# Kernel optimization log

Measured on AMD Instinct MI355X. Metric: run time of the kernel, lower is better.

The kernel has to match this reference:

```python
import jax, jax.numpy as jnp
import numpy as np

N = 50000
E = 600000
IN_DIM = 256
OUT_DIM = 128
SCALE = 1.8
K = 2
ALPHA = 0.15
EPS = 1e-12  # matches F.normalize eps


def setup_inputs() -> dict:
    key = jax.random.key(0)
    k1, k2, k3, k4 = jax.random.split(key, 4)
    x = jax.random.normal(k1, (N, IN_DIM), dtype=jnp.float32)
    edge_index = jax.random.randint(k2, (2, E), 0, N, dtype=jnp.int64)
    # nn.Linear params (Kaiming-uniform-ish init scale)
    lim = 1.0 / np.sqrt(IN_DIM)
    W = jax.random.uniform(k3, (OUT_DIM, IN_DIM), dtype=jnp.float32, minval=-lim, maxval=lim)
    b = jax.random.uniform(k4, (OUT_DIM,), dtype=jnp.float32, minval=-lim, maxval=lim)
    return {"x": x, "edge_index": edge_index, "W": W, "b": b}


def _gcn_norm(edge_index, num_nodes):
    # add self loops, symmetric normalization D^-1/2 A D^-1/2
    loops = jnp.arange(num_nodes, dtype=edge_index.dtype)
    row = jnp.concatenate([edge_index[0], loops])  # source
    col = jnp.concatenate([edge_index[1], loops])  # target
    deg = jax.ops.segment_sum(jnp.ones_like(col, dtype=jnp.float32), col,
                              num_segments=num_nodes)
    dinv = jnp.where(deg > 0, jax.lax.rsqrt(deg), 0.0)
    w = dinv[row] * dinv[col]
    return row, col, w


def reference(x, edge_index, W, b):
    # linear
    h = x @ W.T + b  # [N, OUT_DIM]
    # L2 normalize over feature dim, then scale
    nrm = jnp.sqrt(jnp.sum(h * h, axis=1, keepdims=True))
    h = h / jnp.maximum(nrm, EPS) * SCALE
    # APPNP propagation (eval mode: edge dropout disabled)
    row, col, w = _gcn_norm(edge_index, N)
    z = h
    for _ in range(K):
        msg = w[:, None] * z[row]  # gather + weight, [E+N, OUT_DIM]
        agg = jax.ops.segment_sum(msg, col, num_segments=N)
        z = (1.0 - ALPHA) * agg + ALPHA * h
    return z
```

## Files before the change

### kernel.cpp

```cpp
#include <hip/hip_runtime.h>
#include <hip/hip_bf16.h>

#define NNODES 50000
#define IN_DIM 256
#define OUT_DIM 128
#define SCALE 1.8f
#define ALPHA 0.15f
#define NB_SCAN 196

typedef unsigned short ushort_t;
typedef __attribute__((ext_vector_type(8))) _Float16 f16x8;
typedef __attribute__((ext_vector_type(4))) float f32x4;


__device__ __forceinline__ unsigned short f2bf_rne(float f) {
    unsigned int u = __float_as_uint(f);
    unsigned int r = u + 0x7fffu + ((u >> 16) & 1u);
    return (unsigned short)(r >> 16);
}

__device__ __forceinline__ float2 bf2_to_f2(unsigned int p) {
    float2 f;
    f.x = __uint_as_float(p << 16);
    f.y = __uint_as_float(p & 0xffff0000u);
    return f;
}

__device__ __forceinline__ unsigned int f2_to_bf2(float x, float y) {
    return (unsigned int)f2bf_rne(x) | ((unsigned int)f2bf_rne(y) << 16);
}

__device__ __forceinline__ unsigned short f2h(float f) {
    _Float16 h = (_Float16)f;
    return *(unsigned short*)&h;
}


__global__ void deg_scatter_kernel(const int* __restrict__ col, int* __restrict__ cnt, int E) {
    int e = blockIdx.x * blockDim.x + threadIdx.x;
    if (e < E) atomicAdd(&cnt[col[e]], 1);
}


__global__ void wcvt_kernel(const float* __restrict__ W, ushort_t* __restrict__ Whf) {
    int i = blockIdx.x * blockDim.x + threadIdx.x;
    if (i < OUT_DIM * IN_DIM) Whf[i] = f2h(W[i]);
}


__global__ void scan_pass1(const int* __restrict__ cnt, int* __restrict__ part) {
    __shared__ int sd[256];
    int t = threadIdx.x;
    int i = blockIdx.x * 256 + t;
    sd[t] = (i < NNODES) ? cnt[i] : 0;
    __syncthreads();
    for (int s = 128; s > 0; s >>= 1) {
        if (t < s) sd[t] += sd[t + s];
        __syncthreads();
    }
    if (t == 0) part[blockIdx.x] = sd[0];
}

__global__ void scan_pass2(int* __restrict__ part) {
    __shared__ int s[256];
    int t = threadIdx.x;
    int v = (t < NB_SCAN) ? part[t] : 0;
    s[t] = v;
    __syncthreads();
    for (int o = 1; o < 256; o <<= 1) {
        int u = (t >= o) ? s[t - o] : 0;
        __syncthreads();
        s[t] += u;
        __syncthreads();
    }
    if (t < NB_SCAN) part[t] = (t == 0) ? 0 : s[t - 1];
}

__global__ void scan_pass3(const int* __restrict__ cnt, const int* __restrict__ part,
                           int* __restrict__ off, int* __restrict__ cur,
                           float* __restrict__ dinv, float* __restrict__ q,
                           float2* __restrict__ gr, int E) {
    __shared__ int s[256];
    int t = threadIdx.x;
    int i = blockIdx.x * 256 + t;
    int v = (i < NNODES) ? cnt[i] : 0;
    s[t] = v;
    __syncthreads();
    for (int o = 1; o < 256; o <<= 1) {
        int u = (t >= o) ? s[t - o] : 0;
        __syncthreads();
        s[t] += u;
        __syncthreads();
    }
    int excl = part[blockIdx.x] + ((t == 0) ? 0 : s[t - 1]);
    if (i < NNODES) {
        off[i] = excl;
        cur[i] = excl;
        float deg = (float)(v + 1);
        float d = rsqrtf(deg);
        dinv[i] = d;
        q[i] = (1.0f - ALPHA) * d * d;
        gr[i] = make_float2((1.0f - ALPHA) * d, ALPHA * sqrtf(deg));
    }
    if (i == NNODES - 1) off[NNODES] = E;
}

__global__ void csr_fill_kernel(const int* __restrict__ row, const int* __restrict__ col,
                                int* __restrict__ cur, int* __restrict__ csr_row, int E) {
    int e = blockIdx.x * blockDim.x + threadIdx.x;
    if (e < E) {
        int c = col[e];
        int p = atomicAdd(&cur[c], 1);
        csr_row[p] = row[e];
    }
}


#define XPAD 264

__global__ void __launch_bounds__(256, 4) gemm_norm_kernel(
        const float* __restrict__ x, const ushort_t* __restrict__ Whf,
        const float* __restrict__ b, const float* __restrict__ dinv,
        ushort_t* __restrict__ s0b) {
    __shared__ __align__(16) ushort_t xh[64][XPAD];

    const int t = threadIdx.x;
    const int wv = t >> 6;
    const int lane = t & 63;
    const int q = lane >> 4;
    const int c = lane & 15;
    const int rowBase = blockIdx.x * 64;

    f16x8 wf[2][8];
    float bias[2];
    #pragma unroll
    for (int j = 0; j < 2; ++j) {
        const size_t base = (size_t)((2 * wv + j) * 16 + c) * IN_DIM + q * 8;
        #pragma unroll
        for (int kt = 0; kt < 8; ++kt)
            wf[j][kt] = *(const f16x8*)(Whf + base + kt * 32);
        bias[j] = b[(2 * wv + j) * 16 + c];
    }

    #pragma unroll
    for (int it = 0; it < 16; ++it) {
        int s = it * 256 + t;
        int r = s >> 6;
        int ks = (s & 63) * 4;
        int grow = rowBase + r;
        float4 v = make_float4(0.f, 0.f, 0.f, 0.f);
        if (grow < NNODES) v = *(const float4*)(x + (size_t)grow * IN_DIM + ks);
        uint2 p;
        p.x = (unsigned int)f2h(v.x) | ((unsigned int)f2h(v.y) << 16);
        p.y = (unsigned int)f2h(v.z) | ((unsigned int)f2h(v.w) << 16);
        *(uint2*)&xh[r][ks] = p;
    }
    __syncthreads();

    f32x4 acc[4][2];
    #pragma unroll
    for (int m = 0; m < 4; ++m)
        #pragma unroll
        for (int j = 0; j < 2; ++j) {
            acc[m][j][0] = bias[j]; acc[m][j][1] = bias[j];
            acc[m][j][2] = bias[j]; acc[m][j][3] = bias[j];
        }

    #pragma unroll
    for (int kt = 0; kt < 8; ++kt) {
        const int kb = kt * 32 + q * 8;
        #pragma unroll
        for (int m = 0; m < 4; ++m) {
            f16x8 a = *(const f16x8*)&xh[m * 16 + c][kb];
            #pragma unroll
            for (int j = 0; j < 2; ++j)
                acc[m][j] = __builtin_amdgcn_mfma_f32_16x16x32_f16(a, wf[j][kt], acc[m][j], 0, 0, 0);
        }
    }

    float psum[4][4];
    #pragma unroll
    for (int m = 0; m < 4; ++m)
        #pragma unroll
        for (int r = 0; r < 4; ++r)
            psum[m][r] = acc[m][0][r] * acc[m][0][r] + acc[m][1][r] * acc[m][1][r];
    #pragma unroll
    for (int mask = 1; mask < 16; mask <<= 1)
        #pragma unroll
        for (int m = 0; m < 4; ++m)
            #pragma unroll
            for (int r = 0; r < 4; ++r)
                psum[m][r] += __shfl_xor(psum[m][r], mask);

    __syncthreads();
    float* red = (float*)&xh[0][0];
    float* scl = red + 64 * 8;
    if (c == 0) {
        #pragma unroll
        for (int m = 0; m < 4; ++m)
            #pragma unroll
            for (int r = 0; r < 4; ++r)
                red[(m * 16 + q * 4 + r) * 8 + wv] = psum[m][r];
    }
    __syncthreads();
    if (t < 64) {
        float s = red[t * 8 + 0] + red[t * 8 + 1] + red[t * 8 + 2] + red[t * 8 + 3];
        scl[t] = dinv[rowBase + t] * SCALE / fmaxf(sqrtf(s), 1e-12f);
    }
    __syncthreads();

    #pragma unroll
    for (int m = 0; m < 4; ++m) {
        #pragma unroll
        for (int r = 0; r < 4; ++r) {
            int lrow = m * 16 + q * 4 + r;
            int grow = rowBase + lrow;
            if (grow < NNODES) {
                float sc = scl[lrow];
                #pragma unroll
                for (int j = 0; j < 2; ++j) {
                    float o = acc[m][j][r] * sc;
                    s0b[(size_t)grow * OUT_DIM + (2 * wv + j) * 16 + c] = f2bf_rne(o);
                }
            }
        }
    }
}


__device__ __forceinline__ void acc_row4(float2* a, uint4 v) {
    float2 f0 = bf2_to_f2(v.x), f1 = bf2_to_f2(v.y);
    float2 f2 = bf2_to_f2(v.z), f3 = bf2_to_f2(v.w);
    a[0].x += f0.x; a[0].y += f0.y;
    a[1].x += f1.x; a[1].y += f1.y;
    a[2].x += f2.x; a[2].y += f2.y;
    a[3].x += f3.x; a[3].y += f3.y;
}

template <int FINAL>
__global__ void __launch_bounds__(256) gather_kernel(
        const int* __restrict__ off, const int* __restrict__ csr_row,
        const float* __restrict__ q, const float2* __restrict__ gr,
        const unsigned int* __restrict__ sin, const unsigned int* __restrict__ s0,
        unsigned int* __restrict__ sout_b, float* __restrict__ out_f) {
    const int wv = threadIdx.x >> 6;
    const int lane = threadIdx.x & 63;
    const int qd = lane >> 4;
    const int d16 = lane & 15;
    const int c = blockIdx.x * 4 + wv;

    const int s = off[c];
    const int e = off[c + 1];

    float2 a[4];
    #pragma unroll
    for (int k = 0; k < 4; ++k) a[k] = make_float2(0.f, 0.f);

    for (int base = s; base < e; base += 64) {
        int n = e - base;
        if (n > 64) n = 64;
        int idx = 0;
        if (lane < n) idx = csr_row[base + lane];
        int j = 0;
        for (; j + 8 <= n; j += 8) {
            int r0 = __shfl(idx, j + qd);
            int r1 = __shfl(idx, j + 4 + qd);
            uint4 v0 = *(const uint4*)(sin + (size_t)r0 * 64 + d16 * 4);
            uint4 v1 = *(const uint4*)(sin + (size_t)r1 * 64 + d16 * 4);
            acc_row4(a, v0);
            acc_row4(a, v1);
        }
        for (; j < n; j += 4) {
            int jj = j + qd;
            int r0 = __shfl(idx, (jj < n) ? jj : (n - 1));
            if (jj < n) {
                uint4 v0 = *(const uint4*)(sin + (size_t)r0 * 64 + d16 * 4);
                acc_row4(a, v0);
            }
        }
    }

    #pragma unroll
    for (int k = 0; k < 4; ++k) {
        a[k].x += __shfl_xor(a[k].x, 16);
        a[k].y += __shfl_xor(a[k].y, 16);
        a[k].x += __shfl_xor(a[k].x, 32);
        a[k].y += __shfl_xor(a[k].y, 32);
    }

    if (qd == 0) {
        uint4 zc4 = *(const uint4*)(sin + (size_t)c * 64 + d16 * 4);
        float2 zc[4];
        zc[0] = bf2_to_f2(zc4.x); zc[1] = bf2_to_f2(zc4.y);
        zc[2] = bf2_to_f2(zc4.z); zc[3] = bf2_to_f2(zc4.w);
        #pragma unroll
        for (int k = 0; k < 4; ++k) {
            a[k].x += zc[k].x;
            a[k].y += zc[k].y;
        }
        if (FINAL) {
            uint4 z04 = *(const uint4*)(s0 + (size_t)c * 64 + d16 * 4);
            float2 z0[4];
            z0[0] = bf2_to_f2(z04.x); z0[1] = bf2_to_f2(z04.y);
            z0[2] = bf2_to_f2(z04.z); z0[3] = bf2_to_f2(z04.w);
            float2 g = gr[c];
            float4 o0, o1;
            o0.x = g.x * a[0].x + g.y * z0[0].x;
            o0.y = g.x * a[0].y + g.y * z0[0].y;
            o0.z = g.x * a[1].x + g.y * z0[1].x;
            o0.w = g.x * a[1].y + g.y * z0[1].y;
            o1.x = g.x * a[2].x + g.y * z0[2].x;
            o1.y = g.x * a[2].y + g.y * z0[2].y;
            o1.z = g.x * a[3].x + g.y * z0[3].x;
            o1.w = g.x * a[3].y + g.y * z0[3].y;
            float* p = out_f + (size_t)c * 128 + d16 * 8;
            *(float4*)(p) = o0;
            *(float4*)(p + 4) = o1;
        } else {
            float qc = q[c];
            uint4 w;
            w.x = f2_to_bf2(qc * a[0].x + ALPHA * zc[0].x, qc * a[0].y + ALPHA * zc[0].y);
            w.y = f2_to_bf2(qc * a[1].x + ALPHA * zc[1].x, qc * a[1].y + ALPHA * zc[1].y);
            w.z = f2_to_bf2(qc * a[2].x + ALPHA * zc[2].x, qc * a[2].y + ALPHA * zc[2].y);
            w.w = f2_to_bf2(qc * a[3].x + ALPHA * zc[3].x, qc * a[3].y + ALPHA * zc[3].y);
            *(uint4*)(sout_b + (size_t)c * 64 + d16 * 4) = w;
        }
    }
}

extern "C" void kernel_launch(void* const* d_in, const int* in_sizes, int n_in,
                              void* d_out, int out_size, void* d_ws, size_t ws_size,
                              hipStream_t stream) {
    const float* x  = (const float*)d_in[0];
    const int*   ei = (const int*)d_in[1];
    const float* W  = (const float*)d_in[2];
    const float* b  = (const float*)d_in[3];
    float* out = (float*)d_out;

    int E = in_sizes[1] / 2;
    const int* row = ei;
    const int* col = ei + E;

    float*  dinv = (float*)d_ws;
    float*  q    = dinv + 50048;
    float2* gr   = (float2*)(q + 50048);
    unsigned int* s0b = (unsigned int*)(gr + 50048);
    unsigned int* s1b = s0b + (size_t)NNODES * 64;
    int*   cnt   = (int*)(s1b + (size_t)NNODES * 64);
    int*   off   = cnt + 50048;
    int*   cur   = off + 50112;
    int*   part  = cur + 50048;
    int*   csr_row = part + 256;
    ushort_t* Whf  = (ushort_t*)(csr_row + ((E + 63) & ~63));

    hipMemsetAsync(cnt, 0, NNODES * sizeof(int), stream);
    deg_scatter_kernel<<<(E + 255) / 256, 256, 0, stream>>>(col, cnt, E);
    wcvt_kernel<<<(OUT_DIM * IN_DIM + 255) / 256, 256, 0, stream>>>(W, Whf);

    scan_pass1<<<NB_SCAN, 256, 0, stream>>>(cnt, part);
    scan_pass2<<<1, 256, 0, stream>>>(part);
    scan_pass3<<<NB_SCAN, 256, 0, stream>>>(cnt, part, off, cur, dinv, q, gr, E);
    csr_fill_kernel<<<(E + 255) / 256, 256, 0, stream>>>(row, col, cur, csr_row, E);

    gemm_norm_kernel<<<(NNODES + 63) / 64, 256, 0, stream>>>(x, Whf, b, dinv, (ushort_t*)s0b);

    gather_kernel<0><<<NNODES / 4, 256, 0, stream>>>(off, csr_row, q, gr, s0b, s0b, s1b, nullptr);
    gather_kernel<1><<<NNODES / 4, 256, 0, stream>>>(off, csr_row, q, gr, s1b, s0b, nullptr, out);
}
```

Baseline: 232.3 us.

## Merge graph preprocessing kernels into one cooperative kernel with grid syncs

Replaces the memset, degree scatter, weight conversion, three-pass scan and CSR fill launches with a single cooperative kernel of 1024 blocks that separates the phases with grid.sync(). The aim is to remove per-launch overhead and the idle gaps between the many small dependent kernels. In exchange, the scatter loops become grid-strided over fewer threads, each grid barrier has its own cost, and the kernel depends on all 1024 blocks being co-resident for the cooperative launch.

```diff
diff --git a/kernel.cpp b/kernel.cpp
--- a/kernel.cpp
+++ b/kernel.cpp
@@ -1,5 +1,8 @@
 #include <hip/hip_runtime.h>
 #include <hip/hip_bf16.h>
+#include <hip/hip_cooperative_groups.h>
+
+namespace cg = cooperative_groups;
 
 #define NNODES 50000
 #define IN_DIM 256
@@ -36,79 +39,79 @@
 }
 
 
-__global__ void deg_scatter_kernel(const int* __restrict__ col, int* __restrict__ cnt, int E) {
-    int e = blockIdx.x * blockDim.x + threadIdx.x;
-    if (e < E) atomicAdd(&cnt[col[e]], 1);
-}
-
-
-__global__ void wcvt_kernel(const float* __restrict__ W, ushort_t* __restrict__ Whf) {
-    int i = blockIdx.x * blockDim.x + threadIdx.x;
-    if (i < OUT_DIM * IN_DIM) Whf[i] = f2h(W[i]);
-}
-
-
-__global__ void scan_pass1(const int* __restrict__ cnt, int* __restrict__ part) {
+__global__ void __launch_bounds__(256, 4) prep_coop(
+        const int* __restrict__ row, const int* __restrict__ col, int E,
+        const float* __restrict__ W, ushort_t* __restrict__ Whf,
+        int* __restrict__ cnt, int* __restrict__ part,
+        int* __restrict__ off, int* __restrict__ cur,
+        float* __restrict__ dinv, float* __restrict__ q,
+        float2* __restrict__ gr, int* __restrict__ csr_row) {
+    cg::grid_group grid = cg::this_grid();
     __shared__ int sd[256];
-    int t = threadIdx.x;
-    int i = blockIdx.x * 256 + t;
-    sd[t] = (i < NNODES) ? cnt[i] : 0;
-    __syncthreads();
-    for (int s = 128; s > 0; s >>= 1) {
-        if (t < s) sd[t] += sd[t + s];
+
+    const int t = threadIdx.x;
+    const int gid = blockIdx.x * 256 + t;
+    const int gsz = gridDim.x * 256;
+
+    for (int i = gid; i < NNODES; i += gsz) cnt[i] = 0;
+    for (int i = gid; i < OUT_DIM * IN_DIM; i += gsz) Whf[i] = f2h(W[i]);
+    grid.sync();
+
+    for (int e = gid; e < E; e += gsz) atomicAdd(&cnt[col[e]], 1);
+    grid.sync();
+
+    if (blockIdx.x < NB_SCAN) {
+        int i = blockIdx.x * 256 + t;
+        sd[t] = (i < NNODES) ? cnt[i] : 0;
         __syncthreads();
-    }
-    if (t == 0) part[blockIdx.x] = sd[0];
-}
-
-__global__ void scan_pass2(int* __restrict__ part) {
-    __shared__ int s[256];
-    int t = threadIdx.x;
-    int v = (t < NB_SCAN) ? part[t] : 0;
-    s[t] = v;
-    __syncthreads();
-    for (int o = 1; o < 256; o <<= 1) {
-        int u = (t >= o) ? s[t - o] : 0;
+        for (int s = 128; s > 0; s >>= 1) {
+            if (t < s) sd[t] += sd[t + s];
+            __syncthreads();
+        }
+        if (t == 0) part[blockIdx.x] = sd[0];
+    }
+    grid.sync();
+
+    if (blockIdx.x == 0) {
+        int v = (t < NB_SCAN) ? part[t] : 0;
+        sd[t] = v;
         __syncthreads();
-        s[t] += u;
+        for (int o = 1; o < 256; o <<= 1) {
+            int u = (t >= o) ? sd[t - o] : 0;
+            __syncthreads();
+            sd[t] += u;
+            __syncthreads();
+        }
+        if (t < NB_SCAN) part[t] = (t == 0) ? 0 : sd[t - 1];
+    }
+    grid.sync();
+
+    if (blockIdx.x < NB_SCAN) {
+        int i = blockIdx.x * 256 + t;
+        int v = (i < NNODES) ? cnt[i] : 0;
+        sd[t] = v;
         __syncthreads();
-    }
-    if (t < NB_SCAN) part[t] = (t == 0) ? 0 : s[t - 1];
-}
-
-__global__ void scan_pass3(const int* __restrict__ cnt, const int* __restrict__ part,
-                           int* __restrict__ off, int* __restrict__ cur,
-                           float* __restrict__ dinv, float* __restrict__ q,
-                           float2* __restrict__ gr, int E) {
-    __shared__ int s[256];
-    int t = threadIdx.x;
-    int i = blockIdx.x * 256 + t;
-    int v = (i < NNODES) ? cnt[i] : 0;
-    s[t] = v;
-    __syncthreads();
-    for (int o = 1; o < 256; o <<= 1) {
-        int u = (t >= o) ? s[t - o] : 0;
-        __syncthreads();
-        s[t] += u;
-        __syncthreads();
-    }
-    int excl = part[blockIdx.x] + ((t == 0) ? 0 : s[t - 1]);
-    if (i < NNODES) {
-        off[i] = excl;
-        cur[i] = excl;
-        float deg = (float)(v + 1);
-        float d = rsqrtf(deg);
-        dinv[i] = d;
-        q[i] = (1.0f - ALPHA) * d * d;
-        gr[i] = make_float2((1.0f - ALPHA) * d, ALPHA * sqrtf(deg));
-    }
-    if (i == NNODES - 1) off[NNODES] = E;
-}
-
-__global__ void csr_fill_kernel(const int* __restrict__ row, const int* __restrict__ col,
-                                int* __restrict__ cur, int* __restrict__ csr_row, int E) {
-    int e = blockIdx.x * blockDim.x + threadIdx.x;
-    if (e < E) {
+        for (int o = 1; o < 256; o <<= 1) {
+            int u = (t >= o) ? sd[t - o] : 0;
+            __syncthreads();
+            sd[t] += u;
+            __syncthreads();
+        }
+        int excl = part[blockIdx.x] + ((t == 0) ? 0 : sd[t - 1]);
+        if (i < NNODES) {
+            off[i] = excl;
+            cur[i] = excl;
+            float deg = (float)(v + 1);
+            float d = rsqrtf(deg);
+            dinv[i] = d;
+            q[i] = (1.0f - ALPHA) * d * d;
+            gr[i] = make_float2((1.0f - ALPHA) * d, ALPHA * sqrtf(deg));
+        }
+        if (i == NNODES - 1) off[NNODES] = E;
+    }
+    grid.sync();
+
+    for (int e = gid; e < E; e += gsz) {
         int c = col[e];
         int p = atomicAdd(&cur[c], 1);
         csr_row[p] = row[e];
@@ -353,14 +356,17 @@
     int*   csr_row = part + 256;
     ushort_t* Whf  = (ushort_t*)(csr_row + ((E + 63) & ~63));
 
-    hipMemsetAsync(cnt, 0, NNODES * sizeof(int), stream);
-    deg_scatter_kernel<<<(E + 255) / 256, 256, 0, stream>>>(col, cnt, E);
-    wcvt_kernel<<<(OUT_DIM * IN_DIM + 255) / 256, 256, 0, stream>>>(W, Whf);
-
-    scan_pass1<<<NB_SCAN, 256, 0, stream>>>(cnt, part);
-    scan_pass2<<<1, 256, 0, stream>>>(part);
-    scan_pass3<<<NB_SCAN, 256, 0, stream>>>(cnt, part, off, cur, dinv, q, gr, E);
-    csr_fill_kernel<<<(E + 255) / 256, 256, 0, stream>>>(row, col, cur, csr_row, E);
+    {
+        void* args[] = {
+            (void*)&row, (void*)&col, (void*)&E,
+            (void*)&W, (void*)&Whf,
+            (void*)&cnt, (void*)&part,
+            (void*)&off, (void*)&cur,
+            (void*)&dinv, (void*)&q, (void*)&gr, (void*)&csr_row
+        };
+        hipLaunchCooperativeKernel(reinterpret_cast<void*>(prep_coop),
+                                   dim3(1024), dim3(256), args, 0, stream);
+    }
 
     gemm_norm_kernel<<<(NNODES + 63) / 64, 256, 0, stream>>>(x, Whf, b, dinv, (ushort_t*)s0b);
 
```

New measurement: 710.7 us. 206% more time.
